# Optimization experiments

Hardware: AMD Instinct MI355X
Metric: run time of the kernel (lower is better)

The kernel has to match this reference:

```python
import jax, jax.numpy as jnp
import numpy as np

T, NI, NK, F, H, O, E = 8, 20000, 50000, 128, 256, 128, 500000


def setup_inputs() -> dict:
    key = jax.random.key(0)
    ks = jax.random.split(key, 32)
    s = 0.05
    inp = {
        "x_inf": jax.random.normal(ks[0], (T, NI, F), jnp.float32),
        "x_item": jax.random.normal(ks[1], (T, NK, F), jnp.float32),
        "e1_src": jax.random.randint(ks[2], (T, E), 0, NI, jnp.int32),
        "e1_dst": jax.random.randint(ks[3], (T, E), 0, NK, jnp.int32),
        "e2_src": jax.random.randint(ks[4], (T, E), 0, NK, jnp.int32),
        "e2_dst": jax.random.randint(ks[5], (T, E), 0, NI, jnp.int32),
        "target_idx": 1234,
        # layer 1, edge type a: influencer -> item (dst = item)
        "W1a_l": s * jax.random.normal(ks[6], (H, F), jnp.float32),
        "b1a_l": jnp.zeros((H,), jnp.float32),
        "W1a_r": s * jax.random.normal(ks[7], (H, F), jnp.float32),
        # layer 1, edge type b: item -> influencer (dst = influencer)
        "W1b_l": s * jax.random.normal(ks[8], (H, F), jnp.float32),
        "b1b_l": jnp.zeros((H,), jnp.float32),
        "W1b_r": s * jax.random.normal(ks[9], (H, F), jnp.float32),
        # layer 2, edge type a (dst = item; output unused by the model head, grads are zero)
        "W2a_l": s * jax.random.normal(ks[10], (O, H), jnp.float32),
        "b2a_l": jnp.zeros((O,), jnp.float32),
        "W2a_r": s * jax.random.normal(ks[11], (O, H), jnp.float32),
        # layer 2, edge type b (dst = influencer)
        "W2b_l": s * jax.random.normal(ks[12], (O, H), jnp.float32),
        "b2b_l": jnp.zeros((O,), jnp.float32),
        "W2b_r": s * jax.random.normal(ks[13], (O, H), jnp.float32),
        # GRU (PyTorch gate order: r, z, n)
        "W_ih": s * jax.random.normal(ks[14], (3 * H, O), jnp.float32),
        "W_hh": s * jax.random.normal(ks[15], (3 * H, H), jnp.float32),
        "b_ih": jnp.zeros((3 * H,), jnp.float32),
        "b_hh": jnp.zeros((3 * H,), jnp.float32),
        # attention + prediction head
        "W_att": s * jax.random.normal(ks[16], (1, H), jnp.float32),
        "b_att": jnp.zeros((1,), jnp.float32),
        "W_p1": s * jax.random.normal(ks[17], (H // 2, H), jnp.float32),
        "b_p1": jnp.zeros((H // 2,), jnp.float32),
        "W_p2": s * jax.random.normal(ks[18], (1, H // 2), jnp.float32),
        "b_p2": jnp.zeros((1,), jnp.float32),
    }
    return inp


def _sage(x_src, x_dst, src, dst, Wl, bl, Wr, n_dst):
    # PyG SAGEConv: lin_l(mean_j x_j) + lin_r(x_i); lin_l has bias, lin_r does not
    msg = x_src[src]                                            # [E, F]
    agg = jax.ops.segment_sum(msg, dst, num_segments=n_dst)     # [n_dst, F]
    cnt = jax.ops.segment_sum(jnp.ones_like(dst, dtype=x_src.dtype), dst, num_segments=n_dst)
    mean = agg / jnp.maximum(cnt, 1.0)[:, None]
    return mean @ Wl.T + bl + x_dst @ Wr.T


def reference(x_inf, x_item, e1_src, e1_dst, e2_src, e2_dst, target_idx,
              W1a_l, b1a_l, W1a_r, W1b_l, b1b_l, W1b_r,
              W2a_l, b2a_l, W2a_r, W2b_l, b2b_l, W2b_r,
              W_ih, W_hh, b_ih, b_hh, W_att, b_att, W_p1, b_p1, W_p2, b_p2):
    def step(carry, xs):
        xi, xk, s1, d1, s2, d2 = xs
        # hetero conv1 (aggr='sum' over edge types; each dst type has one incoming edge type)
        h_item = jax.nn.relu(_sage(xi, xk, s1, d1, W1a_l, b1a_l, W1a_r, NK))
        h_inf = jax.nn.relu(_sage(xk, xi, s2, d2, W1b_l, b1b_l, W1b_r, NI))
        # conv2: only the influencer output feeds the head (item output is dead code)
        o_inf = _sage(h_item, h_inf, s2, d2, W2b_l, b2b_l, W2b_r, NI)
        return carry, o_inf[target_idx]

    _, seq = jax.lax.scan(step, None, (x_inf, x_item, e1_src, e1_dst, e2_src, e2_dst))  # [T, O]

    def gru_step(h, x):
        gi = x @ W_ih.T + b_ih
        gh = h @ W_hh.T + b_hh
        i_r, i_z, i_n = jnp.split(gi, 3)
        h_r, h_z, h_n = jnp.split(gh, 3)
        r = jax.nn.sigmoid(i_r + h_r)
        z = jax.nn.sigmoid(i_z + h_z)
        n = jnp.tanh(i_n + r * h_n)
        h_new = (1.0 - z) * n + z * h
        return h_new, h_new

    h0 = jnp.zeros((H,), seq.dtype)
    _, rnn = jax.lax.scan(gru_step, h0, seq)                    # [T, H]

    att = jax.nn.softmax(rnn @ W_att.T + b_att, axis=0)         # [T, 1]
    ctx = jnp.sum(att * rnn, axis=0)                            # [H]
    hid = jax.nn.relu(ctx @ W_p1.T + b_p1)
    score = (hid @ W_p2.T + b_p2)[0]
    return score
```

## Files before the change

### kernel.cpp

```cpp
#include <hip/hip_runtime.h>
#include <math.h>

#define T 8
#define NI 20000
#define NK 50000
#define F 128
#define H 256
#define O 128
#define E 500000
#define G3 (3*H)
#define MAXS 256
#define BMW 1568
#define NB 8
#define RPB 32

#define OFF_CNT2   0
#define OFF_ITEMS  32
#define OFF_CNT1   (32 + T*MAXS*4)
#define OFF_SUMX2  (OFF_CNT1 + T*MAXS*4)
#define OFF_HSUM   (OFF_SUMX2 + T*F*4)
#define OFF_O      (OFF_HSUM + T*H*4)
#define OFF_GI     (OFF_O + T*O*4)
#define OFF_RNN    (OFF_GI + T*G3*4)
#define OFF_BAR    (OFF_RNN + T*H*4)
#define OFF_SUM1   (OFF_BAR + 64)
#define WS_USED    (OFF_SUM1 + (size_t)T*MAXS*F*4)

__global__ void k_find_e2(const int* __restrict__ e2_src, const int* __restrict__ e2_dst,
                          const float* __restrict__ x_item, const int* __restrict__ target_p,
                          int* __restrict__ cnt2, int* __restrict__ items,
                          float* __restrict__ sum_x2) {
    int t = blockIdx.y;
    long j = (long)blockIdx.x * 256 + threadIdx.x;
    if (j >= E) return;
    int target = *target_p;
    if (e2_dst[(long)t * E + j] == target) {
        int src = e2_src[(long)t * E + j];
        int pos = atomicAdd(&cnt2[t], 1);
        if (pos < MAXS) items[t * MAXS + pos] = src;
        const float* xr = x_item + ((long)t * NK + src) * F;
        float* acc = sum_x2 + t * F;
        for (int f = 0; f < F; ++f) atomicAdd(&acc[f], xr[f]);
    }
}

__global__ void k_scan_e1(const int* __restrict__ e1_src, const int* __restrict__ e1_dst,
                          const float* __restrict__ x_inf,
                          const int* __restrict__ cnt2, const int* __restrict__ items,
                          int* __restrict__ cnt1, float* __restrict__ sum1) {
    __shared__ int s_items[MAXS];
    __shared__ unsigned s_bm[BMW];
    int t = blockIdx.y;
    int ns = min(cnt2[t], MAXS);
    for (int i = threadIdx.x; i < BMW; i += 256) s_bm[i] = 0u;
    __syncthreads();
    for (int i = threadIdx.x; i < ns; i += 256) {
        int it = items[t * MAXS + i];
        s_items[i] = it;
        atomicOr(&s_bm[it >> 5], 1u << (it & 31));
    }
    __syncthreads();
    long j = (long)blockIdx.x * 256 + threadIdx.x;
    if (j >= E) return;
    int d = e1_dst[(long)t * E + j];
    if (!((s_bm[d >> 5] >> (d & 31)) & 1u)) return;
    int src = e1_src[(long)t * E + j];
    const float* xr = x_inf + ((long)t * NI + src) * F;
    for (int i = 0; i < ns; ++i) {
        if (s_items[i] == d) {
            atomicAdd(&cnt1[t * MAXS + i], 1);
            float* acc = sum1 + ((long)t * MAXS + i) * F;
            for (int f = 0; f < F; ++f) atomicAdd(&acc[f], xr[f]);
        }
    }
}

__global__ void k_hitem(const float* __restrict__ x_item,
                        const float* __restrict__ W1a_l, const float* __restrict__ b1a_l,
                        const float* __restrict__ W1a_r,
                        const int* __restrict__ cnt2, const int* __restrict__ items,
                        const int* __restrict__ cnt1, const float* __restrict__ sum1,
                        float* __restrict__ hsum) {
    int t = blockIdx.y, slot = blockIdx.x;
    int ns = min(cnt2[t], MAXS);
    if (slot >= ns) return;
    __shared__ float z1[F], xk[F];
    int item = items[t * MAXS + slot];
    float inv = 1.0f / fmaxf((float)cnt1[t * MAXS + slot], 1.0f);
    if (threadIdx.x < F) {
        z1[threadIdx.x] = sum1[((long)t * MAXS + slot) * F + threadIdx.x] * inv;
        xk[threadIdx.x] = x_item[((long)t * NK + item) * F + threadIdx.x];
    }
    __syncthreads();
    int h = threadIdx.x;
    float acc = b1a_l[h];
    const float* wl = W1a_l + h * F;
    const float* wr = W1a_r + h * F;
    for (int f = 0; f < F; ++f) acc += z1[f] * wl[f] + xk[f] * wr[f];
    acc = fmaxf(acc, 0.0f);
    atomicAdd(&hsum[t * H + h], acc);
}

__global__ void k_layer2(const float* __restrict__ x_inf, const int* __restrict__ target_p,
                         const float* __restrict__ W1b_l, const float* __restrict__ b1b_l,
                         const float* __restrict__ W1b_r,
                         const float* __restrict__ W2b_l, const float* __restrict__ b2b_l,
                         const float* __restrict__ W2b_r,
                         const int* __restrict__ cnt2, const float* __restrict__ sum_x2,
                         const float* __restrict__ hsum, float* __restrict__ o) {
    int t = blockIdx.x;
    __shared__ float z2[F], xt[F], hinf[H], mh[H];
    int target = *target_p;
    float c2 = fmaxf((float)cnt2[t], 1.0f);
    if (threadIdx.x < F) {
        z2[threadIdx.x] = sum_x2[t * F + threadIdx.x] / c2;
        xt[threadIdx.x] = x_inf[((long)t * NI + target) * F + threadIdx.x];
    }
    __syncthreads();
    int h = threadIdx.x;
    {
        float acc = b1b_l[h];
        const float* wl = W1b_l + h * F;
        const float* wr = W1b_r + h * F;
        for (int f = 0; f < F; ++f) acc += z2[f] * wl[f] + xt[f] * wr[f];
        hinf[h] = fmaxf(acc, 0.0f);
        mh[h] = hsum[t * H + h] / c2;
    }
    __syncthreads();
    if (threadIdx.x < O) {
        int f = threadIdx.x;
        float acc = b2b_l[f];
        const float* wl = W2b_l + f * H;
        const float* wr = W2b_r + f * H;
        for (int k = 0; k < H; ++k) acc += mh[k] * wl[k] + hinf[k] * wr[k];
        o[t * O + f] = acc;
    }
}

__global__ void k_gi(const float* __restrict__ o, const float* __restrict__ W_ih,
                     const float* __restrict__ b_ih, float* __restrict__ gi) {
    int t = blockIdx.y;
    int wv = threadIdx.x >> 6, lane = threadIdx.x & 63;
    int row = blockIdx.x * 4 + wv;
    const float* w = W_ih + (long)row * O;
    const float* x = o + t * O;
    float s = w[lane] * x[lane] + w[lane + 64] * x[lane + 64];
    for (int off = 32; off; off >>= 1) s += __shfl_down(s, off);
    if (lane == 0) gi[t * G3 + row] = s + b_ih[row];
}

__global__ void __launch_bounds__(256, 1)
k_gru(const float* __restrict__ gi, const float* __restrict__ W_hh,
      const float* __restrict__ b_hh,
      const float* __restrict__ W_att, const float* __restrict__ b_att,
      const float* __restrict__ W_p1, const float* __restrict__ b_p1,
      const float* __restrict__ W_p2, const float* __restrict__ b_p2,
      float* __restrict__ rnn, int* __restrict__ bar, float* __restrict__ out) {
    __shared__ float w[3 * RPB][H];
    __shared__ float h[H];
    __shared__ float srnn[T][H];
    __shared__ float satt[T], tmp[H], hid[128];
    int b = blockIdx.x, tid = threadIdx.x;
    for (int idx = tid; idx < 3 * RPB * H; idx += 256) {
        int r = idx >> 8, k = idx & 255;
        int g = r / RPB, j = r - g * RPB;
        w[r][k] = W_hh[((long)(g * H + b * RPB + j)) * H + k];
    }
    h[tid] = 0.0f;
    __syncthreads();
    int wv = tid >> 6, lane = tid & 63;
    for (int t = 0; t < T; ++t) {
        for (int j = wv; j < RPB; j += 4) {
            float sr = 0.f, sz = 0.f, sn = 0.f;
            for (int c = 0; c < 4; ++c) {
                int k = lane + 64 * c;
                float hk = h[k];
                sr += w[j][k] * hk;
                sz += w[RPB + j][k] * hk;
                sn += w[2 * RPB + j][k] * hk;
            }
            for (int off = 32; off; off >>= 1) {
                sr += __shfl_down(sr, off);
                sz += __shfl_down(sz, off);
                sn += __shfl_down(sn, off);
            }
            if (lane == 0) {
                int i = b * RPB + j;
                float gir = gi[t * G3 + i];
                float giz = gi[t * G3 + H + i];
                float gin = gi[t * G3 + 2 * H + i];
                float r = 1.0f / (1.0f + expf(-(gir + sr + b_hh[i])));
                float z = 1.0f / (1.0f + expf(-(giz + sz + b_hh[H + i])));
                float n = tanhf(gin + r * (sn + b_hh[2 * H + i]));
                float hn = (1.0f - z) * n + z * h[i];
                __hip_atomic_store(&rnn[t * H + i], hn, __ATOMIC_RELAXED,
                                   __HIP_MEMORY_SCOPE_AGENT);
            }
        }
        __syncthreads();
        if (tid == 0) {
            __threadfence();
            __hip_atomic_fetch_add(&bar[t], 1, __ATOMIC_RELEASE, __HIP_MEMORY_SCOPE_AGENT);
            while (__hip_atomic_load(&bar[t], __ATOMIC_ACQUIRE, __HIP_MEMORY_SCOPE_AGENT) < NB)
                __builtin_amdgcn_s_sleep(1);
            __threadfence();
        }
        __syncthreads();
        h[tid] = __hip_atomic_load(&rnn[t * H + tid], __ATOMIC_RELAXED,
                                   __HIP_MEMORY_SCOPE_AGENT);
        __syncthreads();
    }
    if (b != 0) return;
    for (int idx = tid; idx < T * H; idx += 256)
        srnn[idx >> 8][idx & 255] = __hip_atomic_load(&rnn[idx], __ATOMIC_RELAXED,
                                                      __HIP_MEMORY_SCOPE_AGENT);
    __syncthreads();
    {
        int tt = tid >> 5, l32 = tid & 31;
        float a = 0.f;
        for (int c = 0; c < 8; ++c) {
            int k = l32 + 32 * c;
            a += W_att[k] * srnn[tt][k];
        }
        for (int off = 16; off; off >>= 1) a += __shfl_down(a, off, 32);
        if (l32 == 0) satt[tt] = a + b_att[0];
    }
    __syncthreads();
    if (tid == 0) {
        float m = satt[0];
        for (int t = 1; t < T; ++t) m = fmaxf(m, satt[t]);
        float s = 0.f;
        for (int t = 0; t < T; ++t) { satt[t] = expf(satt[t] - m); s += satt[t]; }
        for (int t = 0; t < T; ++t) satt[t] /= s;
    }
    __syncthreads();
    {
        float ctx = 0.f;
        for (int t = 0; t < T; ++t) ctx += satt[t] * srnn[t][tid];
        tmp[tid] = ctx;
    }
    __syncthreads();
    if (tid < 128) {
        float a = b_p1[tid];
        const float* wp = W_p1 + (long)tid * H;
        for (int k = 0; k < H; ++k) a += wp[k] * tmp[k];
        hid[tid] = fmaxf(a, 0.0f);
    }
    __syncthreads();
    if (tid == 0) {
        float s = b_p2[0];
        for (int k = 0; k < 128; ++k) s += W_p2[k] * hid[k];
        out[0] = s;
    }
}

extern "C" void kernel_launch(void* const* d_in, const int* in_sizes, int n_in,
                              void* d_out, int out_size, void* d_ws, size_t ws_size,
                              hipStream_t stream) {
    const float* x_inf  = (const float*)d_in[0];
    const float* x_item = (const float*)d_in[1];
    const int* e1_src = (const int*)d_in[2];
    const int* e1_dst = (const int*)d_in[3];
    const int* e2_src = (const int*)d_in[4];
    const int* e2_dst = (const int*)d_in[5];
    const int* target_p = (const int*)d_in[6];
    const float* W1a_l = (const float*)d_in[7];
    const float* b1a_l = (const float*)d_in[8];
    const float* W1a_r = (const float*)d_in[9];
    const float* W1b_l = (const float*)d_in[10];
    const float* b1b_l = (const float*)d_in[11];
    const float* W1b_r = (const float*)d_in[12];
    const float* W2b_l = (const float*)d_in[16];
    const float* b2b_l = (const float*)d_in[17];
    const float* W2b_r = (const float*)d_in[18];
    const float* W_ih = (const float*)d_in[19];
    const float* W_hh = (const float*)d_in[20];
    const float* b_ih = (const float*)d_in[21];
    const float* b_hh = (const float*)d_in[22];
    const float* W_att = (const float*)d_in[23];
    const float* b_att = (const float*)d_in[24];
    const float* W_p1 = (const float*)d_in[25];
    const float* b_p1 = (const float*)d_in[26];
    const float* W_p2 = (const float*)d_in[27];
    const float* b_p2 = (const float*)d_in[28];
    float* out = (float*)d_out;

    char* ws = (char*)d_ws;
    int*   cnt2   = (int*)(ws + OFF_CNT2);
    int*   items  = (int*)(ws + OFF_ITEMS);
    int*   cnt1   = (int*)(ws + OFF_CNT1);
    float* sum_x2 = (float*)(ws + OFF_SUMX2);
    float* hsum   = (float*)(ws + OFF_HSUM);
    float* o      = (float*)(ws + OFF_O);
    float* gi     = (float*)(ws + OFF_GI);
    float* rnn    = (float*)(ws + OFF_RNN);
    int*   bar    = (int*)(ws + OFF_BAR);
    float* sum1   = (float*)(ws + OFF_SUM1);

    hipMemsetAsync(d_ws, 0, WS_USED, stream);

    dim3 g1((E + 255) / 256, T);
    k_find_e2<<<g1, 256, 0, stream>>>(e2_src, e2_dst, x_item, target_p, cnt2, items, sum_x2);

    dim3 g2((E + 255) / 256, T);
    k_scan_e1<<<g2, 256, 0, stream>>>(e1_src, e1_dst, x_inf, cnt2, items, cnt1, sum1);

    dim3 g3(MAXS, T);
    k_hitem<<<g3, 256, 0, stream>>>(x_item, W1a_l, b1a_l, W1a_r, cnt2, items, cnt1, sum1, hsum);

    k_layer2<<<T, 256, 0, stream>>>(x_inf, target_p, W1b_l, b1b_l, W1b_r,
                                    W2b_l, b2b_l, W2b_r, cnt2, sum_x2, hsum, o);

    dim3 g5(G3 / 4, T);
    k_gi<<<g5, 256, 0, stream>>>(o, W_ih, b_ih, gi);

    k_gru<<<NB, 256, 0, stream>>>(gi, W_hh, b_hh, W_att, b_att,
                                  W_p1, b_p1, W_p2, b_p2, rnn, bar, out);
}
```

Before: 676.8 us.

## Fuse item, layer2, input-gate and GRU stages into one persistent kernel with flag barriers

The k_hitem, k_layer2, k_gi and k_gru kernels are merged into one 8-block persistent kernel. Cross-block dependencies are handled with per-phase flag barriers in global memory instead of separate launches. The edge-scan kernels now read destination indices as int4, so each thread checks four edges. This removes four kernel launches and their gaps. In exchange, the h_item stage runs on only 8 blocks instead of up to 256×T, which serialises that work.

```diff
diff --git a/kernel.cpp b/kernel.cpp
--- a/kernel.cpp
+++ b/kernel.cpp
@@ -13,17 +13,17 @@
 #define BMW 1568
 #define NB 8
 #define RPB 32
+#define NPHASE 10
 
 #define OFF_CNT2   0
 #define OFF_ITEMS  32
-#define OFF_CNT1   (32 + T*MAXS*4)
+#define OFF_CNT1   (OFF_ITEMS + T*MAXS*4)
 #define OFF_SUMX2  (OFF_CNT1 + T*MAXS*4)
 #define OFF_HSUM   (OFF_SUMX2 + T*F*4)
-#define OFF_O      (OFF_HSUM + T*H*4)
-#define OFF_GI     (OFF_O + T*O*4)
+#define OFF_GI     (OFF_HSUM + T*H*4)
 #define OFF_RNN    (OFF_GI + T*G3*4)
-#define OFF_BAR    (OFF_RNN + T*H*4)
-#define OFF_SUM1   (OFF_BAR + 64)
+#define OFF_FLAGS  (OFF_RNN + T*H*4)
+#define OFF_SUM1   (OFF_FLAGS + NPHASE*NB*16*4)
 #define WS_USED    (OFF_SUM1 + (size_t)T*MAXS*F*4)
 
 __global__ void k_find_e2(const int* __restrict__ e2_src, const int* __restrict__ e2_dst,
@@ -31,16 +31,22 @@
                           int* __restrict__ cnt2, int* __restrict__ items,
                           float* __restrict__ sum_x2) {
     int t = blockIdx.y;
-    long j = (long)blockIdx.x * 256 + threadIdx.x;
-    if (j >= E) return;
+    long q = (long)blockIdx.x * 256 + threadIdx.x;
+    if (q >= E / 4) return;
     int target = *target_p;
-    if (e2_dst[(long)t * E + j] == target) {
-        int src = e2_src[(long)t * E + j];
-        int pos = atomicAdd(&cnt2[t], 1);
-        if (pos < MAXS) items[t * MAXS + pos] = src;
-        const float* xr = x_item + ((long)t * NK + src) * F;
-        float* acc = sum_x2 + t * F;
-        for (int f = 0; f < F; ++f) atomicAdd(&acc[f], xr[f]);
+    int4 d4 = ((const int4*)(e2_dst + (long)t * E))[q];
+    int dv[4] = {d4.x, d4.y, d4.z, d4.w};
+    #pragma unroll
+    for (int c = 0; c < 4; ++c) {
+        if (dv[c] == target) {
+            long j = q * 4 + c;
+            int src = e2_src[(long)t * E + j];
+            int pos = atomicAdd(&cnt2[t], 1);
+            if (pos < MAXS) items[t * MAXS + pos] = src;
+            const float* xr = x_item + ((long)t * NK + src) * F;
+            float* acc = sum_x2 + t * F;
+            for (int f = 0; f < F; ++f) atomicAdd(&acc[f], xr[f]);
+        }
     }
 }
 
@@ -60,113 +66,134 @@
         atomicOr(&s_bm[it >> 5], 1u << (it & 31));
     }
     __syncthreads();
-    long j = (long)blockIdx.x * 256 + threadIdx.x;
-    if (j >= E) return;
-    int d = e1_dst[(long)t * E + j];
-    if (!((s_bm[d >> 5] >> (d & 31)) & 1u)) return;
-    int src = e1_src[(long)t * E + j];
-    const float* xr = x_inf + ((long)t * NI + src) * F;
-    for (int i = 0; i < ns; ++i) {
-        if (s_items[i] == d) {
-            atomicAdd(&cnt1[t * MAXS + i], 1);
-            float* acc = sum1 + ((long)t * MAXS + i) * F;
-            for (int f = 0; f < F; ++f) atomicAdd(&acc[f], xr[f]);
-        }
-    }
-}
-
-__global__ void k_hitem(const float* __restrict__ x_item,
-                        const float* __restrict__ W1a_l, const float* __restrict__ b1a_l,
-                        const float* __restrict__ W1a_r,
-                        const int* __restrict__ cnt2, const int* __restrict__ items,
-                        const int* __restrict__ cnt1, const float* __restrict__ sum1,
-                        float* __restrict__ hsum) {
-    int t = blockIdx.y, slot = blockIdx.x;
-    int ns = min(cnt2[t], MAXS);
-    if (slot >= ns) return;
+    long q = (long)blockIdx.x * 256 + threadIdx.x;
+    if (q >= E / 4) return;
+    int4 d4 = ((const int4*)(e1_dst + (long)t * E))[q];
+    int dv[4] = {d4.x, d4.y, d4.z, d4.w};
+    #pragma unroll
+    for (int c = 0; c < 4; ++c) {
+        int d = dv[c];
+        if (!((s_bm[d >> 5] >> (d & 31)) & 1u)) continue;
+        int src = e1_src[(long)t * E + q * 4 + c];
+        const float* xr = x_inf + ((long)t * NI + src) * F;
+        for (int i = 0; i < ns; ++i) {
+            if (s_items[i] == d) {
+                atomicAdd(&cnt1[t * MAXS + i], 1);
+                float* acc = sum1 + ((long)t * MAXS + i) * F;
+                for (int f = 0; f < F; ++f) atomicAdd(&acc[f], xr[f]);
+            }
+        }
+    }
+}
+
+__device__ __forceinline__ void flag_barrier(int* flags, int phase, int b) {
+    __syncthreads();
+    int tid = threadIdx.x;
+    if (tid == 0) {
+        __threadfence();
+        __hip_atomic_store(&flags[(phase * NB + b) * 16], 1, __ATOMIC_RELEASE,
+                           __HIP_MEMORY_SCOPE_AGENT);
+    }
+    if (tid < NB) {
+        while (__hip_atomic_load(&flags[(phase * NB + tid) * 16], __ATOMIC_ACQUIRE,
+                                 __HIP_MEMORY_SCOPE_AGENT) == 0)
+            __builtin_amdgcn_s_sleep(1);
+        __threadfence();
+    }
+    __syncthreads();
+}
+
+__global__ void __launch_bounds__(256, 1)
+k_fused(const float* __restrict__ x_item, const float* __restrict__ x_inf,
+        const int* __restrict__ target_p,
+        const float* __restrict__ W1a_l, const float* __restrict__ b1a_l,
+        const float* __restrict__ W1a_r,
+        const float* __restrict__ W1b_l, const float* __restrict__ b1b_l,
+        const float* __restrict__ W1b_r,
+        const float* __restrict__ W2b_l, const float* __restrict__ b2b_l,
+        const float* __restrict__ W2b_r,
+        const float* __restrict__ W_ih, const float* __restrict__ b_ih,
+        const float* __restrict__ W_hh, const float* __restrict__ b_hh,
+        const float* __restrict__ W_att, const float* __restrict__ b_att,
+        const float* __restrict__ W_p1, const float* __restrict__ b_p1,
+        const float* __restrict__ W_p2, const float* __restrict__ b_p2,
+        const int* __restrict__ cnt2, const int* __restrict__ items,
+        const int* __restrict__ cnt1, const float* __restrict__ sum_x2,
+        const float* __restrict__ sum1,
+        float* __restrict__ hsum, float* __restrict__ gi, float* __restrict__ rnn,
+        int* __restrict__ flags, float* __restrict__ out) {
+    __shared__ float w[3 * RPB][H];
     __shared__ float z1[F], xk[F];
-    int item = items[t * MAXS + slot];
-    float inv = 1.0f / fmaxf((float)cnt1[t * MAXS + slot], 1.0f);
-    if (threadIdx.x < F) {
-        z1[threadIdx.x] = sum1[((long)t * MAXS + slot) * F + threadIdx.x] * inv;
-        xk[threadIdx.x] = x_item[((long)t * NK + item) * F + threadIdx.x];
-    }
-    __syncthreads();
-    int h = threadIdx.x;
-    float acc = b1a_l[h];
-    const float* wl = W1a_l + h * F;
-    const float* wr = W1a_r + h * F;
-    for (int f = 0; f < F; ++f) acc += z1[f] * wl[f] + xk[f] * wr[f];
-    acc = fmaxf(acc, 0.0f);
-    atomicAdd(&hsum[t * H + h], acc);
-}
-
-__global__ void k_layer2(const float* __restrict__ x_inf, const int* __restrict__ target_p,
-                         const float* __restrict__ W1b_l, const float* __restrict__ b1b_l,
-                         const float* __restrict__ W1b_r,
-                         const float* __restrict__ W2b_l, const float* __restrict__ b2b_l,
-                         const float* __restrict__ W2b_r,
-                         const int* __restrict__ cnt2, const float* __restrict__ sum_x2,
-                         const float* __restrict__ hsum, float* __restrict__ o) {
-    int t = blockIdx.x;
-    __shared__ float z2[F], xt[F], hinf[H], mh[H];
-    int target = *target_p;
-    float c2 = fmaxf((float)cnt2[t], 1.0f);
-    if (threadIdx.x < F) {
-        z2[threadIdx.x] = sum_x2[t * F + threadIdx.x] / c2;
-        xt[threadIdx.x] = x_inf[((long)t * NI + target) * F + threadIdx.x];
-    }
-    __syncthreads();
-    int h = threadIdx.x;
-    {
-        float acc = b1b_l[h];
-        const float* wl = W1b_l + h * F;
-        const float* wr = W1b_r + h * F;
-        for (int f = 0; f < F; ++f) acc += z2[f] * wl[f] + xt[f] * wr[f];
-        hinf[h] = fmaxf(acc, 0.0f);
-        mh[h] = hsum[t * H + h] / c2;
-    }
-    __syncthreads();
-    if (threadIdx.x < O) {
-        int f = threadIdx.x;
-        float acc = b2b_l[f];
-        const float* wl = W2b_l + f * H;
-        const float* wr = W2b_r + f * H;
-        for (int k = 0; k < H; ++k) acc += mh[k] * wl[k] + hinf[k] * wr[k];
-        o[t * O + f] = acc;
-    }
-}
-
-__global__ void k_gi(const float* __restrict__ o, const float* __restrict__ W_ih,
-                     const float* __restrict__ b_ih, float* __restrict__ gi) {
-    int t = blockIdx.y;
-    int wv = threadIdx.x >> 6, lane = threadIdx.x & 63;
-    int row = blockIdx.x * 4 + wv;
-    const float* w = W_ih + (long)row * O;
-    const float* x = o + t * O;
-    float s = w[lane] * x[lane] + w[lane + 64] * x[lane + 64];
-    for (int off = 32; off; off >>= 1) s += __shfl_down(s, off);
-    if (lane == 0) gi[t * G3 + row] = s + b_ih[row];
-}
-
-__global__ void __launch_bounds__(256, 1)
-k_gru(const float* __restrict__ gi, const float* __restrict__ W_hh,
-      const float* __restrict__ b_hh,
-      const float* __restrict__ W_att, const float* __restrict__ b_att,
-      const float* __restrict__ W_p1, const float* __restrict__ b_p1,
-      const float* __restrict__ W_p2, const float* __restrict__ b_p2,
-      float* __restrict__ rnn, int* __restrict__ bar, float* __restrict__ out) {
-    __shared__ float w[3 * RPB][H];
-    __shared__ float h[H];
+    __shared__ float hvec[H];
     __shared__ float srnn[T][H];
-    __shared__ float satt[T], tmp[H], hid[128];
+    __shared__ float satt[T], tmp[H], hid[H / 2];
     int b = blockIdx.x, tid = threadIdx.x;
+
     for (int idx = tid; idx < 3 * RPB * H; idx += 256) {
         int r = idx >> 8, k = idx & 255;
         int g = r / RPB, j = r - g * RPB;
         w[r][k] = W_hh[((long)(g * H + b * RPB + j)) * H + k];
     }
-    h[tid] = 0.0f;
+
+    for (int t = 0; t < T; ++t) {
+        int ns = min(cnt2[t], MAXS);
+        for (int s = b; s < ns; s += NB) {
+            __syncthreads();
+            if (tid < F) {
+                int item = items[t * MAXS + s];
+                float inv = 1.0f / fmaxf((float)cnt1[t * MAXS + s], 1.0f);
+                z1[tid] = sum1[((long)t * MAXS + s) * F + tid] * inv;
+                xk[tid] = x_item[((long)t * NK + item) * F + tid];
+            }
+            __syncthreads();
+            float acc = b1a_l[tid];
+            const float* wl = W1a_l + tid * F;
+            const float* wr = W1a_r + tid * F;
+            for (int f = 0; f < F; ++f) acc += z1[f] * wl[f] + xk[f] * wr[f];
+            atomicAdd(&hsum[t * H + tid], fmaxf(acc, 0.0f));
+        }
+    }
+    flag_barrier(flags, 0, b);
+
+    {
+        int t = b;
+        int target = *target_p;
+        float c2 = fmaxf((float)cnt2[t], 1.0f);
+        __syncthreads();
+        if (tid < F) {
+            z1[tid] = sum_x2[t * F + tid] / c2;
+            xk[tid] = x_inf[((long)t * NI + target) * F + tid];
+        }
+        __syncthreads();
+        float acc = b1b_l[tid];
+        {
+            const float* wl = W1b_l + tid * F;
+            const float* wr = W1b_r + tid * F;
+            for (int f = 0; f < F; ++f) acc += z1[f] * wl[f] + xk[f] * wr[f];
+        }
+        hvec[tid] = fmaxf(acc, 0.0f);
+        tmp[tid] = hsum[t * H + tid] / c2;
+        __syncthreads();
+        if (tid < O) {
+            float a = b2b_l[tid];
+            const float* wl = W2b_l + tid * H;
+            const float* wr = W2b_r + tid * H;
+            for (int k = 0; k < H; ++k) a += tmp[k] * wl[k] + hvec[k] * wr[k];
+            z1[tid] = a;
+        }
+        __syncthreads();
+        for (int r = 0; r < 3; ++r) {
+            int row = tid + r * 256;
+            float a = b_ih[row];
+            const float* wi = W_ih + (long)row * O;
+            for (int k = 0; k < O; ++k) a += wi[k] * z1[k];
+            __hip_atomic_store(&gi[t * G3 + row], a, __ATOMIC_RELAXED,
+                               __HIP_MEMORY_SCOPE_AGENT);
+        }
+    }
+    flag_barrier(flags, 1, b);
+
+    hvec[tid] = 0.0f;
     __syncthreads();
     int wv = tid >> 6, lane = tid & 63;
     for (int t = 0; t < T; ++t) {
@@ -174,7 +201,7 @@
             float sr = 0.f, sz = 0.f, sn = 0.f;
             for (int c = 0; c < 4; ++c) {
                 int k = lane + 64 * c;
-                float hk = h[k];
+                float hk = hvec[k];
                 sr += w[j][k] * hk;
                 sz += w[RPB + j][k] * hk;
                 sn += w[2 * RPB + j][k] * hk;
@@ -186,35 +213,29 @@
             }
             if (lane == 0) {
                 int i = b * RPB + j;
-                float gir = gi[t * G3 + i];
-                float giz = gi[t * G3 + H + i];
-                float gin = gi[t * G3 + 2 * H + i];
+                float gir = __hip_atomic_load(&gi[t * G3 + i], __ATOMIC_RELAXED,
+                                              __HIP_MEMORY_SCOPE_AGENT);
+                float giz = __hip_atomic_load(&gi[t * G3 + H + i], __ATOMIC_RELAXED,
+                                              __HIP_MEMORY_SCOPE_AGENT);
+                float gin = __hip_atomic_load(&gi[t * G3 + 2 * H + i], __ATOMIC_RELAXED,
+                                              __HIP_MEMORY_SCOPE_AGENT);
                 float r = 1.0f / (1.0f + expf(-(gir + sr + b_hh[i])));
                 float z = 1.0f / (1.0f + expf(-(giz + sz + b_hh[H + i])));
                 float n = tanhf(gin + r * (sn + b_hh[2 * H + i]));
-                float hn = (1.0f - z) * n + z * h[i];
+                float hn = (1.0f - z) * n + z * hvec[i];
                 __hip_atomic_store(&rnn[t * H + i], hn, __ATOMIC_RELAXED,
                                    __HIP_MEMORY_SCOPE_AGENT);
             }
         }
-        __syncthreads();
-        if (tid == 0) {
-            __threadfence();
-            __hip_atomic_fetch_add(&bar[t], 1, __ATOMIC_RELEASE, __HIP_MEMORY_SCOPE_AGENT);
-            while (__hip_atomic_load(&bar[t], __ATOMIC_ACQUIRE, __HIP_MEMORY_SCOPE_AGENT) < NB)
-                __builtin_amdgcn_s_sleep(1);
-            __threadfence();
-        }
-        __syncthreads();
-        h[tid] = __hip_atomic_load(&rnn[t * H + tid], __ATOMIC_RELAXED,
-                                   __HIP_MEMORY_SCOPE_AGENT);
+        flag_barrier(flags, 2 + t, b);
+        float hnew = __hip_atomic_load(&rnn[t * H + tid], __ATOMIC_RELAXED,
+                                       __HIP_MEMORY_SCOPE_AGENT);
+        hvec[tid] = hnew;
+        if (b == 0) srnn[t][tid] = hnew;
         __syncthreads();
     }
     if (b != 0) return;
-    for (int idx = tid; idx < T * H; idx += 256)
-        srnn[idx >> 8][idx & 255] = __hip_atomic_load(&rnn[idx], __ATOMIC_RELAXED,
-                                                      __HIP_MEMORY_SCOPE_AGENT);
-    __syncthreads();
+
     {
         int tt = tid >> 5, l32 = tid & 31;
         float a = 0.f;
@@ -240,7 +261,7 @@
         tmp[tid] = ctx;
     }
     __syncthreads();
-    if (tid < 128) {
+    if (tid < H / 2) {
         float a = b_p1[tid];
         const float* wp = W_p1 + (long)tid * H;
         for (int k = 0; k < H; ++k) a += wp[k] * tmp[k];
@@ -249,7 +270,7 @@
     __syncthreads();
     if (tid == 0) {
         float s = b_p2[0];
-        for (int k = 0; k < 128; ++k) s += W_p2[k] * hid[k];
+        for (int k = 0; k < H / 2; ++k) s += W_p2[k] * hid[k];
         out[0] = s;
     }
 }
@@ -291,29 +312,23 @@
     int*   cnt1   = (int*)(ws + OFF_CNT1);
     float* sum_x2 = (float*)(ws + OFF_SUMX2);
     float* hsum   = (float*)(ws + OFF_HSUM);
-    float* o      = (float*)(ws + OFF_O);
     float* gi     = (float*)(ws + OFF_GI);
     float* rnn    = (float*)(ws + OFF_RNN);
-    int*   bar    = (int*)(ws + OFF_BAR);
+    int*   flags  = (int*)(ws + OFF_FLAGS);
     float* sum1   = (float*)(ws + OFF_SUM1);
 
     hipMemsetAsync(d_ws, 0, WS_USED, stream);
 
-    dim3 g1((E + 255) / 256, T);
+    dim3 g1((E / 4 + 255) / 256, T);
     k_find_e2<<<g1, 256, 0, stream>>>(e2_src, e2_dst, x_item, target_p, cnt2, items, sum_x2);
-
-    dim3 g2((E + 255) / 256, T);
-    k_scan_e1<<<g2, 256, 0, stream>>>(e1_src, e1_dst, x_inf, cnt2, items, cnt1, sum1);
-
-    dim3 g3(MAXS, T);
-    k_hitem<<<g3, 256, 0, stream>>>(x_item, W1a_l, b1a_l, W1a_r, cnt2, items, cnt1, sum1, hsum);
-
-    k_layer2<<<T, 256, 0, stream>>>(x_inf, target_p, W1b_l, b1b_l, W1b_r,
-                                    W2b_l, b2b_l, W2b_r, cnt2, sum_x2, hsum, o);
-
-    dim3 g5(G3 / 4, T);
-    k_gi<<<g5, 256, 0, stream>>>(o, W_ih, b_ih, gi);
-
-    k_gru<<<NB, 256, 0, stream>>>(gi, W_hh, b_hh, W_att, b_att,
-                                  W_p1, b_p1, W_p2, b_p2, rnn, bar, out);
-}
+    k_scan_e1<<<g1, 256, 0, stream>>>(e1_src, e1_dst, x_inf, cnt2, items, cnt1, sum1);
+
+    k_fused<<<NB, 256, 0, stream>>>(x_item, x_inf, target_p,
+                                    W1a_l, b1a_l, W1a_r,
+                                    W1b_l, b1b_l, W1b_r,
+                                    W2b_l, b2b_l, W2b_r,
+                                    W_ih, b_ih, W_hh, b_hh,
+                                    W_att, b_att, W_p1, b_p1, W_p2, b_p2,
+                                    cnt2, items, cnt1, sum_x2, sum1,
+                                    hsum, gi, rnn, flags, out);
+}
```

New measurement: 960.1 us. 41.9% more time.
